# Kernel tuning notes

Hardware: AMD Instinct MI355X
Metric: run time of the kernel (lower is better)

## Reference

```python
import math
import jax, jax.numpy as jnp
import numpy as np

B = 128          # graphs per batch
N = 1024         # nodes per graph
E = 1048576      # total edges (avg degree 8)
F_IN = 64
NHID = 64
NCLS = 10
RATIO = 0.8


def setup_inputs() -> dict:
    key = jax.random.key(0)
    ks = jax.random.split(key, 24)
    x = jax.random.normal(ks[0], (B * N, F_IN), jnp.float32)
    # intra-graph random edges: graph id per edge, local src/dst
    epg = E // B
    gid = jnp.repeat(jnp.arange(B, dtype=jnp.int32), epg)
    src = gid * N + jax.random.randint(ks[1], (E,), 0, N, jnp.int32)
    dst = gid * N + jax.random.randint(ks[2], (E,), 0, N, jnp.int32)
    def lin(k, fi, fo):
        s = 1.0 / np.sqrt(fi)
        return jax.random.uniform(k, (fi, fo), jnp.float32, -s, s)
    p = {
        'W1': lin(ks[3], F_IN, NHID), 'b1': jnp.zeros((NHID,), jnp.float32),
        'Wp1': lin(ks[4], NHID, 1), 'bp1': jnp.zeros((1,), jnp.float32),
        'W2': lin(ks[5], NHID, NHID), 'b2': jnp.zeros((NHID,), jnp.float32),
        'Wp2': lin(ks[6], NHID, 1), 'bp2': jnp.zeros((1,), jnp.float32),
        'W3': lin(ks[7], NHID, NHID), 'b3': jnp.zeros((NHID,), jnp.float32),
        'Wp3': lin(ks[8], NHID, 1), 'bp3': jnp.zeros((1,), jnp.float32),
        'L1w': lin(ks[9], 2 * NHID, NHID), 'L1b': jnp.zeros((NHID,), jnp.float32),
        'L2w': lin(ks[10], NHID, NHID // 2), 'L2b': jnp.zeros((NHID // 2,), jnp.float32),
        'L3w': lin(ks[11], NHID // 2, NCLS), 'L3b': jnp.zeros((NCLS,), jnp.float32),
    }
    return dict(x=x, edge_src=src, edge_dst=dst, **p)


def gcn_conv(x, W, b, src, dst, emask, n):
    # PyG GCNConv: add self loops, symmetric deg normalization
    xw = x @ W
    ew = emask.astype(x.dtype)
    deg = jax.ops.segment_sum(ew, dst, num_segments=n) + 1.0  # +1 self loop
    dis = jax.lax.rsqrt(deg)
    norm = dis[src] * dis[dst] * ew
    agg = jax.ops.segment_sum(xw[src] * norm[:, None], dst, num_segments=n)
    agg = agg + xw * (dis * dis)[:, None]  # self-loop message
    return agg + b


def sag_pool(x, Wp, bp, src, dst, emask, n_cur):
    n_tot = B * n_cur
    k = int(math.ceil(RATIO * n_cur))
    score = gcn_conv(x, Wp, bp, src, dst, emask, n_tot)[:, 0]
    _, idx = jax.lax.top_k(score.reshape(B, n_cur), k)
    perm = (idx + (jnp.arange(B, dtype=jnp.int32) * n_cur)[:, None]).reshape(-1)
    xn = x[perm] * jnp.tanh(score[perm])[:, None]
    new_idx = jnp.full((n_tot,), -1, jnp.int32).at[perm].set(
        jnp.arange(B * k, dtype=jnp.int32))
    ns, nd = new_idx[src], new_idx[dst]
    valid = emask & (ns >= 0) & (nd >= 0)
    return xn, jnp.where(valid, ns, 0), jnp.where(valid, nd, 0), valid, k


def readout(x, k):
    xr = x.reshape(B, k, NHID)
    return jnp.concatenate([xr.max(axis=1), xr.mean(axis=1)], axis=1)


def reference(x, edge_src, edge_dst, W1, b1, Wp1, bp1, W2, b2, Wp2, bp2,
              W3, b3, Wp3, bp3, L1w, L1b, L2w, L2b, L3w, L3b):
    src = edge_src.astype(jnp.int32)
    dst = edge_dst.astype(jnp.int32)
    emask = jnp.ones((E,), bool)
    n = N
    h = jax.nn.relu(gcn_conv(x, W1, b1, src, dst, emask, B * n))
    h, src, dst, emask, n = sag_pool(h, Wp1, bp1, src, dst, emask, n)
    r1 = readout(h, n)
    h = jax.nn.relu(gcn_conv(h, W2, b2, src, dst, emask, B * n))
    h, src, dst, emask, n = sag_pool(h, Wp2, bp2, src, dst, emask, n)
    r2 = readout(h, n)
    h = jax.nn.relu(gcn_conv(h, W3, b3, src, dst, emask, B * n))
    h, src, dst, emask, n = sag_pool(h, Wp3, bp3, src, dst, emask, n)
    r3 = readout(h, n)
    z = r1 + r2 + r3
    z = jax.nn.relu(z @ L1w + L1b)          # dropout is identity in eval
    z = jax.nn.relu(z @ L2w + L2b)
    return jax.nn.log_softmax(z @ L3w + L3b, axis=-1)
```

## Files before the change

### kernel.cpp

```cpp
#include <hip/hip_runtime.h>
#include <math.h>

constexpr int B_   = 128;
constexpr int N_   = 1024;
constexpr int E_   = 1048576;
constexpr int BN_  = B_ * N_;
constexpr int EPG  = E_ / B_;
constexpr int SRT2 = EPG + 3 * 1024;
constexpr int NSEG = 16;

typedef short v8s __attribute__((ext_vector_type(8)));
typedef float v4f __attribute__((ext_vector_type(4)));

__device__ __forceinline__ unsigned bf16_rne(unsigned u) {
    return (u + 0x7FFFu + ((u >> 16) & 1u)) >> 16;
}

__global__ __launch_bounds__(1024) void k_csr2(
        const int* __restrict__ src, const int* __restrict__ dst,
        const int* __restrict__ cum,
        int* __restrict__ srt, int* __restrict__ rowptr,
        float* __restrict__ dis, int n) {
    __shared__ int cnt[1024];
    __shared__ int cur[1024];
    __shared__ int cums[1024];
    __shared__ int wsum[17];
    int g = blockIdx.x, tid = threadIdx.x;
    int gb   = g * N_;
    int base = g * n;
    const int eb = g * EPG;
    int* gsrt = srt + (size_t)g * SRT2;

    cums[tid] = cum ? cum[gb + tid] : tid;
    cnt[tid] = 0;
    __syncthreads();
    for (int t = tid; t < EPG; t += 1024) {
        int s = cums[src[eb + t] - gb];
        int d = cums[dst[eb + t] - gb];
        if ((s | d) >= 0) atomicAdd(&cnt[d], 1);
    }
    __syncthreads();

    int c  = (tid < n) ? cnt[tid] : 0;
    int pc = (c + 3) & ~3;
    int v = pc;
    int lane = tid & 63, wv = tid >> 6;
    #pragma unroll
    for (int off = 1; off < 64; off <<= 1) {
        int t = __shfl_up(v, off, 64);
        if (lane >= off) v += t;
    }
    if (lane == 63) wsum[wv] = v;
    __syncthreads();
    if (tid == 0) {
        int run = 0;
        #pragma unroll
        for (int i = 0; i < 16; ++i) { int t = wsum[i]; wsum[i] = run; run += t; }
        wsum[16] = run;
    }
    __syncthreads();
    int excl = v - pc + wsum[wv];
    if (tid < n) {
        cur[tid] = excl;
        rowptr[g * (n + 1) + tid] = excl;
        dis[base + tid] = rsqrtf((float)c + 1.0f);
    }
    if (tid == 0) rowptr[g * (n + 1) + n] = wsum[16];
    __syncthreads();

    for (int t = tid; t < EPG; t += 1024) {
        int s = cums[src[eb + t] - gb];
        int d = cums[dst[eb + t] - gb];
        if ((s | d) < 0) continue;
        int pos = atomicAdd(&cur[d], 1);
        gsrt[pos] = s;
    }
    __syncthreads();

    if (tid < n) {
        int e1 = excl + pc;
        for (int t = cur[tid]; t < e1; ++t) gsrt[t] = n;
    }
}

__global__ __launch_bounds__(1024) void k_wprep3(
        const float* __restrict__ W0, const float* __restrict__ W1,
        const float* __restrict__ W2, unsigned short* __restrict__ wfall) {
    const float* W = (blockIdx.x == 0) ? W0 : (blockIdx.x == 1) ? W1 : W2;
    unsigned short* wf = wfall + (size_t)blockIdx.x * 8192;
    int t = threadIdx.x;
    int l  = t & 63;
    int kk = (t >> 6) & 1;
    int c  = (t >> 7) & 3;
    int p  = (t >> 9) & 1;
    int col = c * 16 + (l & 15);
    int kbase = kk * 32 + (l >> 4) * 8;
    unsigned short o[8];
    #pragma unroll
    for (int j = 0; j < 8; ++j) {
        float w = W[(kbase + j) * 64 + col];
        unsigned u  = __float_as_uint(w);
        unsigned hi = bf16_rne(u);
        if (p == 0) o[j] = (unsigned short)hi;
        else {
            float lo = w - __uint_as_float(hi << 16);
            o[j] = (unsigned short)bf16_rne(__float_as_uint(lo));
        }
    }
    uint4 v;
    v.x = o[0] | ((unsigned)o[1] << 16);
    v.y = o[2] | ((unsigned)o[3] << 16);
    v.z = o[4] | ((unsigned)o[5] << 16);
    v.w = o[6] | ((unsigned)o[7] << 16);
    *reinterpret_cast<uint4*>(wf + (size_t)t * 8) = v;
}

__global__ __launch_bounds__(256) void k_xw_mfma(
        const float* __restrict__ h, const int* __restrict__ perm,
        const float* __restrict__ ggate, const unsigned short* __restrict__ wf,
        const float* __restrict__ dis, float* __restrict__ xwq, int rows) {
    __shared__ float hs[128][68];
    __shared__ float sdis[128];
    __shared__ int   lperm[128];
    __shared__ float lgate[128];
    int tid = threadIdx.x;
    int r0 = blockIdx.x * 128;

    if (perm) {
        if (tid < 128) { lperm[tid] = perm[r0 + tid]; lgate[tid] = ggate[r0 + tid]; }
        __syncthreads();
        for (int i = tid; i < 128 * 16; i += 256) {
            int row = i >> 4, s = i & 15;
            float4 v = *reinterpret_cast<const float4*>(h + (size_t)lperm[row] * 64 + s * 4);
            float gt = lgate[row];
            v.x *= gt; v.y *= gt; v.z *= gt; v.w *= gt;
            *reinterpret_cast<float4*>(&hs[row][s * 4]) = v;
        }
    } else {
        for (int i = tid; i < 128 * 16; i += 256) {
            int row = i >> 4, s = i & 15;
            float4 v = *reinterpret_cast<const float4*>(h + (size_t)(r0 + row) * 64 + s * 4);
            *reinterpret_cast<float4*>(&hs[row][s * 4]) = v;
        }
    }
    if (tid < 128) sdis[tid] = dis[r0 + tid];

    int lane = tid & 63;
    v8s wh[4][2], wl[4][2];
    #pragma unroll
    for (int c = 0; c < 4; ++c) {
        #pragma unroll
        for (int kk = 0; kk < 2; ++kk) {
            wh[c][kk] = *reinterpret_cast<const v8s*>(wf + (((size_t)((0*4 + c)*2 + kk))*64 + lane)*8);
            wl[c][kk] = *reinterpret_cast<const v8s*>(wf + (((size_t)((1*4 + c)*2 + kk))*64 + lane)*8);
        }
    }
    __syncthreads();

    int wave = tid >> 6;
    int m = lane & 15, b = lane >> 4;
    #pragma unroll
    for (int t = 0; t < 2; ++t) {
        int lr0 = (wave * 2 + t) * 16;
        float f[16];
        *reinterpret_cast<float4*>(f)      = *reinterpret_cast<const float4*>(&hs[lr0 + m][b * 8]);
        *reinterpret_cast<float4*>(f + 4)  = *reinterpret_cast<const float4*>(&hs[lr0 + m][b * 8 + 4]);
        *reinterpret_cast<float4*>(f + 8)  = *reinterpret_cast<const float4*>(&hs[lr0 + m][32 + b * 8]);
        *reinterpret_cast<float4*>(f + 12) = *reinterpret_cast<const float4*>(&hs[lr0 + m][32 + b * 8 + 4]);
        v8s ah[2], al[2];
        #pragma unroll
        for (int ch = 0; ch < 2; ++ch) {
            #pragma unroll
            for (int j = 0; j < 8; ++j) {
                float x = f[ch * 8 + j];
                unsigned u  = __float_as_uint(x);
                unsigned hi = bf16_rne(u);
                float lo = x - __uint_as_float(hi << 16);
                ah[ch][j] = (short)hi;
                al[ch][j] = (short)bf16_rne(__float_as_uint(lo));
            }
        }
        float dv[4];
        #pragma unroll
        for (int reg = 0; reg < 4; ++reg) dv[reg] = sdis[lr0 + b * 4 + reg];

        #pragma unroll
        for (int c = 0; c < 4; ++c) {
            v4f acc = {0.f, 0.f, 0.f, 0.f};
            acc = __builtin_amdgcn_mfma_f32_16x16x32_bf16(ah[0], wh[c][0], acc, 0, 0, 0);
            acc = __builtin_amdgcn_mfma_f32_16x16x32_bf16(ah[1], wh[c][1], acc, 0, 0, 0);
            acc = __builtin_amdgcn_mfma_f32_16x16x32_bf16(al[0], wh[c][0], acc, 0, 0, 0);
            acc = __builtin_amdgcn_mfma_f32_16x16x32_bf16(al[1], wh[c][1], acc, 0, 0, 0);
            acc = __builtin_amdgcn_mfma_f32_16x16x32_bf16(ah[0], wl[c][0], acc, 0, 0, 0);
            acc = __builtin_amdgcn_mfma_f32_16x16x32_bf16(ah[1], wl[c][1], acc, 0, 0, 0);
            acc = __builtin_amdgcn_mfma_f32_16x16x32_bf16(al[0], wl[c][0], acc, 0, 0, 0);
            acc = __builtin_amdgcn_mfma_f32_16x16x32_bf16(al[1], wl[c][1], acc, 0, 0, 0);
            #pragma unroll
            for (int reg = 0; reg < 4; ++reg) {
                int grow = r0 + lr0 + b * 4 + reg;
                xwq[((size_t)c * rows + grow) * 16 + m] = acc[reg] * dv[reg];
            }
        }
    }
}

__global__ __launch_bounds__(1024, 1) void k_agg_csr(
        const int* __restrict__ srt, const int* __restrict__ rowptr,
        const float* __restrict__ dis, const float* __restrict__ xwq,
        const float* __restrict__ bias, const float* __restrict__ Wp,
        float* __restrict__ hout, float* __restrict__ saggq,
        int n, int rows) {
    extern __shared__ float xs[];
    int lrpPad = (n + 4) & ~3;
    int* lrp  = (int*)(xs + (n + 1) * 20);
    int* lsrt = lrp + lrpPad;

    int g = blockIdx.x & 127, q = blockIdx.x >> 7;
    int foff = q * 16;
    int tid  = threadIdx.x;
    int base = g * n;
    const float* plane = xwq + ((size_t)q * rows + base) * 16;

    for (int i = tid; i < n * 4; i += 1024) {
        int row = i >> 2, sub = i & 3;
        float4 v = *reinterpret_cast<const float4*>(plane + row * 16 + sub * 4);
        *reinterpret_cast<float4*>(xs + row * 20 + sub * 4) = v;
    }
    if (tid < 20) xs[n * 20 + tid] = 0.0f;
    for (int i = tid; i <= n; i += 1024) lrp[i] = rowptr[g * (n + 1) + i];
    __syncthreads();
    int total = lrp[n];
    const int* gsrt = srt + (size_t)g * SRT2;
    for (int i = tid; i < total; i += 1024) lsrt[i] = gsrt[i];
    __syncthreads();

    int sub = tid & 3;
    float4 bq  = *reinterpret_cast<const float4*>(bias + foff + sub * 4);
    float4 wp4 = *reinterpret_cast<const float4*>(Wp   + foff + sub * 4);
    for (int row = tid >> 2; row < n; row += 256) {
        int s0 = lrp[row], s1 = lrp[row + 1];
        float4 acc = *reinterpret_cast<const float4*>(xs + row * 20 + sub * 4);
        for (int j = s0; j < s1; j += 4) {
            int4 nb = *reinterpret_cast<const int4*>(lsrt + j);
            const float4 v0 = *reinterpret_cast<const float4*>(xs + nb.x * 20 + sub * 4);
            const float4 v1 = *reinterpret_cast<const float4*>(xs + nb.y * 20 + sub * 4);
            const float4 v2 = *reinterpret_cast<const float4*>(xs + nb.z * 20 + sub * 4);
            const float4 v3 = *reinterpret_cast<const float4*>(xs + nb.w * 20 + sub * 4);
            acc.x += v0.x + v1.x + v2.x + v3.x;
            acc.y += v0.y + v1.y + v2.y + v3.y;
            acc.z += v0.z + v1.z + v2.z + v3.z;
            acc.w += v0.w + v1.w + v2.w + v3.w;
        }
        float dsc = dis[base + row];
        float4 o;
        o.x = fmaxf(fmaf(dsc, acc.x, bq.x), 0.0f);
        o.y = fmaxf(fmaf(dsc, acc.y, bq.y), 0.0f);
        o.z = fmaxf(fmaf(dsc, acc.z, bq.z), 0.0f);
        o.w = fmaxf(fmaf(dsc, acc.w, bq.w), 0.0f);
        *reinterpret_cast<float4*>(hout + (size_t)(base + row) * 64 + foff + sub * 4) = o;
        float part = o.x * wp4.x + o.y * wp4.y + o.z * wp4.z + o.w * wp4.w;
        part += __shfl_xor(part, 1, 64);
        part += __shfl_xor(part, 2, 64);
        if (sub == 0) xs[row * 20 + 16] = part * dsc;
    }
    __syncthreads();

    for (int row = tid; row < n; row += 1024) {
        float acc = xs[row * 20 + 16];
        int s1 = lrp[row + 1];
        for (int j = lrp[row]; j < s1; j += 4) {
            int4 nb = *reinterpret_cast<const int4*>(lsrt + j);
            acc += xs[nb.x * 20 + 16] + xs[nb.y * 20 + 16]
                 + xs[nb.z * 20 + 16] + xs[nb.w * 20 + 16];
        }
        saggq[(size_t)q * BN_ + base + row] = acc;
    }
}

__global__ __launch_bounds__(1024) void k_score_topk(
        const float* __restrict__ dis, const float* __restrict__ saggq,
        const float* __restrict__ bp, int n, int k,
        int* __restrict__ perm, float* __restrict__ ggate,
        int* __restrict__ cum, int do_compose) {
    __shared__ unsigned long long keys[1024];
    __shared__ int mark[1024];
    int g = blockIdx.x, tid = threadIdx.x;
    int base = g * n;
    float bp0 = bp[0];

    unsigned long long kv = 0ull;
    if (tid < n) {
        float s0 = saggq[0 * (size_t)BN_ + base + tid] + saggq[1 * (size_t)BN_ + base + tid]
                 + saggq[2 * (size_t)BN_ + base + tid] + saggq[3 * (size_t)BN_ + base + tid];
        float sag = dis[base + tid] * s0 + bp0;
        unsigned u  = __float_as_uint(sag);
        unsigned mk = (u & 0x80000000u) ? ~u : (u | 0x80000000u);
        kv = ((unsigned long long)mk << 32) | (unsigned)tid;
    }
    keys[tid] = kv;
    mark[tid] = -1;

    for (int size = 2; size <= 1024; size <<= 1) {
        for (int stride = size >> 1; stride > 0; stride >>= 1) {
            __syncthreads();
            if (tid < 512) {
                int a  = ((tid / stride) * (stride << 1)) + (tid & (stride - 1));
                int bx = a + stride;
                bool asc = ((a & size) == 0);
                unsigned long long ka = keys[a], kb = keys[bx];
                bool sw = asc ? (ka > kb) : (ka < kb);
                if (sw) { keys[a] = kb; keys[bx] = ka; }
            }
        }
    }
    __syncthreads();

    if (tid < k) {
        int j = tid;
        unsigned long long kvv = keys[1023 - j];
        int local   = (int)(kvv & 0xFFFFFFFFull);
        unsigned mk = (unsigned)(kvv >> 32);
        unsigned u  = (mk & 0x80000000u) ? (mk ^ 0x80000000u) : ~mk;
        int newg = g * k + j;
        perm[newg]  = base + local;
        ggate[newg] = tanhf(__uint_as_float(u));
        mark[local] = j;
    }
    __syncthreads();
    if (do_compose) {
        int gb = g * N_;
        int c = (do_compose == 1) ? tid : cum[gb + tid];
        cum[gb + tid] = (c >= 0) ? mark[c] : -1;
    }
}

__global__ __launch_bounds__(256) void k_readout_seg(
        const float* __restrict__ h, const int* __restrict__ perm,
        const float* __restrict__ ggate, int k, float* __restrict__ pz) {
    int g = blockIdx.x / NSEG, seg = blockIdx.x % NSEG;
    int ck = (k + NSEG - 1) / NSEG;
    int j0 = seg * ck;
    int j1 = min(k, j0 + ck);
    __shared__ float gate[64];
    __shared__ int   lperm[64];
    int tid = threadIdx.x;
    for (int j = j0 + tid; j < j1; j += 256) {
        lperm[j - j0] = perm[g * k + j];
        gate[j - j0]  = ggate[g * k + j];
    }
    __syncthreads();
    int lane = tid & 63, w = tid >> 6;
    float mx = -INFINITY, sm = 0.0f;
    for (int j = j0 + w; j < j1; j += 4) {
        float v = h[(size_t)lperm[j - j0] * 64 + lane] * gate[j - j0];
        mx = fmaxf(mx, v); sm += v;
    }
    __shared__ float smx[4][64], ssm[4][64];
    smx[w][lane] = mx; ssm[w][lane] = sm;
    __syncthreads();
    if (w == 0) {
        #pragma unroll
        for (int i = 1; i < 4; ++i) { mx = fmaxf(mx, smx[i][lane]); sm += ssm[i][lane]; }
        float* p = pz + ((size_t)g * NSEG + seg) * 128;
        p[lane]      = mx;
        p[64 + lane] = sm;
    }
}

__global__ __launch_bounds__(128) void k_mlp(const float* __restrict__ pz,
                      const float* __restrict__ L1w, const float* __restrict__ L1b,
                      const float* __restrict__ L2w, const float* __restrict__ L2b,
                      const float* __restrict__ L3w, const float* __restrict__ L3b,
                      float* __restrict__ out) {
    __shared__ float z[128], h1[64], h2[32], lg[10], lse;
    int g = blockIdx.x, tid = threadIdx.x;
    const float kinv[3] = {1.0f / 820.0f, 1.0f / 656.0f, 1.0f / 525.0f};
    float zv = 0.0f;
    if (tid < 64) {
        #pragma unroll
        for (int L = 0; L < 3; ++L) {
            const float* p = pz + (((size_t)L * B_ + g) * NSEG) * 128;
            float mx = -INFINITY;
            #pragma unroll
            for (int s = 0; s < NSEG; ++s) mx = fmaxf(mx, p[s * 128 + tid]);
            zv += mx;
        }
    } else {
        int f = tid - 64;
        #pragma unroll
        for (int L = 0; L < 3; ++L) {
            const float* p = pz + (((size_t)L * B_ + g) * NSEG) * 128;
            float sm = 0.0f;
            #pragma unroll
            for (int s = 0; s < NSEG; ++s) sm += p[s * 128 + 64 + f];
            zv += sm * kinv[L];
        }
    }
    z[tid] = zv;
    __syncthreads();
    if (tid < 64) {
        float acc = L1b[tid];
        for (int i = 0; i < 128; ++i) acc = fmaf(z[i], L1w[i * 64 + tid], acc);
        h1[tid] = fmaxf(acc, 0.0f);
    }
    __syncthreads();
    if (tid < 32) {
        float acc = L2b[tid];
        for (int i = 0; i < 64; ++i) acc = fmaf(h1[i], L2w[i * 32 + tid], acc);
        h2[tid] = fmaxf(acc, 0.0f);
    }
    __syncthreads();
    if (tid < 10) {
        float acc = L3b[tid];
        for (int i = 0; i < 32; ++i) acc = fmaf(h2[i], L3w[i * 10 + tid], acc);
        lg[tid] = acc;
    }
    __syncthreads();
    if (tid == 0) {
        float m = lg[0];
        for (int i = 1; i < 10; ++i) m = fmaxf(m, lg[i]);
        float s = 0.0f;
        for (int i = 0; i < 10; ++i) s += expf(lg[i] - m);
        lse = m + logf(s);
    }
    __syncthreads();
    if (tid < 10) out[g * 10 + tid] = lg[tid] - lse;
}

extern "C" void kernel_launch(void* const* d_in, const int* in_sizes, int n_in,
                              void* d_out, int out_size, void* d_ws, size_t ws_size,
                              hipStream_t stream) {
    const float* x    = (const float*)d_in[0];
    const int*   esrc = (const int*)d_in[1];
    const int*   edst = (const int*)d_in[2];
    const float* W [3] = {(const float*)d_in[3],  (const float*)d_in[7],  (const float*)d_in[11]};
    const float* bb[3] = {(const float*)d_in[4],  (const float*)d_in[8],  (const float*)d_in[12]};
    const float* Wp[3] = {(const float*)d_in[5],  (const float*)d_in[9],  (const float*)d_in[13]};
    const float* bp[3] = {(const float*)d_in[6],  (const float*)d_in[10], (const float*)d_in[14]};
    const float* L1w = (const float*)d_in[15];
    const float* L1b = (const float*)d_in[16];
    const float* L2w = (const float*)d_in[17];
    const float* L2b = (const float*)d_in[18];
    const float* L3w = (const float*)d_in[19];
    const float* L3b = (const float*)d_in[20];
    float* out = (float*)d_out;

    float* fws   = (float*)d_ws;
    float* agg   = fws;
    float* xwq   = agg  + (size_t)BN_ * 64;
    float* dis   = xwq  + (size_t)BN_ * 64;
    float* saggq = dis  + BN_;
    float* ggate = saggq + 4 * (size_t)BN_;
    float* pz    = ggate + BN_;
    int*   perm   = (int*)(pz + 3 * B_ * NSEG * 128);
    int*   cum    = perm + BN_;
    int*   srt    = cum + BN_;
    int*   rowptr = srt + (size_t)B_ * SRT2;
    unsigned short* wfrag = (unsigned short*)(rowptr + B_ * (N_ + 1));

    hipFuncSetAttribute(reinterpret_cast<const void*>(k_agg_csr),
                        hipFuncAttributeMaxDynamicSharedMemorySize,
                        (1025 * 20 + 1028 + SRT2) * 4);

    k_wprep3<<<3, 1024, 0, stream>>>(W[0], W[1], W[2], wfrag);

    const int ks_[3] = {820, 656, 525};
    int n = N_;

    for (int L = 0; L < 3; ++L) {
        int rows = B_ * n;
        int k    = ks_[L];

        k_csr2<<<B_, 1024, 0, stream>>>(esrc, edst, (L == 0) ? nullptr : cum,
                                        srt, rowptr, dis, n);

        if (L == 0)
            k_xw_mfma<<<rows / 128, 256, 0, stream>>>(x, nullptr, nullptr,
                                                      wfrag, dis, xwq, rows);
        else
            k_xw_mfma<<<rows / 128, 256, 0, stream>>>(agg, perm, ggate,
                                                      wfrag + (size_t)L * 8192, dis, xwq, rows);

        int lrpPad = (n + 4) & ~3;
        k_agg_csr<<<B_ * 4, 1024, (size_t)((n + 1) * 20 + lrpPad + SRT2) * 4, stream>>>(
            srt, rowptr, dis, xwq, bb[L], Wp[L], agg, saggq, n, rows);

        k_score_topk<<<B_, 1024, 0, stream>>>(dis, saggq, bp[L], n, k,
                                              perm, ggate, cum, (L < 2) ? (L + 1) : 0);

        k_readout_seg<<<B_ * NSEG, 256, 0, stream>>>(agg, perm, ggate, k,
                                                     pz + (size_t)L * B_ * NSEG * 128);

        n = k;
    }

    k_mlp<<<B_, 128, 0, stream>>>(pz, L1w, L1b, L2w, L2b, L3w, L3b, out);
}
```

Measured before the change: 262.1 us.

## Split CSR aggregation into eight 8-feature slices with 16-bit neighbor indices

The aggregation kernel now launches 8 blocks per graph, each owning 8 feature columns instead of 16, which cuts the per-block LDS feature tile from 20 to 12 floats per row. Neighbor indices are stored in LDS as unsigned shorts, halving that buffer. The smaller footprint is meant to let more blocks share a CU and to add parallelism. The cost is that each block reloads the whole edge list and row pointers, and the score partial sums grow from 4 to 8 planes, so the top-k kernel reads twice as many.

```diff
diff --git a/kernel.cpp b/kernel.cpp
--- a/kernel.cpp
+++ b/kernel.cpp
@@ -204,48 +204,49 @@
     }
 }
 
-__global__ __launch_bounds__(1024, 1) void k_agg_csr(
+__global__ __launch_bounds__(1024, 8) void k_agg8(
         const int* __restrict__ srt, const int* __restrict__ rowptr,
         const float* __restrict__ dis, const float* __restrict__ xwq,
         const float* __restrict__ bias, const float* __restrict__ Wp,
-        float* __restrict__ hout, float* __restrict__ saggq,
+        float* __restrict__ hout, float* __restrict__ sagg8,
         int n, int rows) {
     extern __shared__ float xs[];
     int lrpPad = (n + 4) & ~3;
-    int* lrp  = (int*)(xs + (n + 1) * 20);
-    int* lsrt = lrp + lrpPad;
-
-    int g = blockIdx.x & 127, q = blockIdx.x >> 7;
-    int foff = q * 16;
+    int* lrp = (int*)(xs + (n + 1) * 12);
+    unsigned short* lsrtU = (unsigned short*)(lrp + lrpPad);
+
+    int g = blockIdx.x & 127, e8 = blockIdx.x >> 7;
+    int q = e8 >> 1, half = (e8 & 1) * 8;
+    int foff = q * 16 + half;
     int tid  = threadIdx.x;
     int base = g * n;
-    const float* plane = xwq + ((size_t)q * rows + base) * 16;
-
-    for (int i = tid; i < n * 4; i += 1024) {
-        int row = i >> 2, sub = i & 3;
-        float4 v = *reinterpret_cast<const float4*>(plane + row * 16 + sub * 4);
-        *reinterpret_cast<float4*>(xs + row * 20 + sub * 4) = v;
-    }
-    if (tid < 20) xs[n * 20 + tid] = 0.0f;
+    const float* plane = xwq + ((size_t)q * rows + base) * 16 + half;
+
+    for (int i = tid; i < n * 2; i += 1024) {
+        int row = i >> 1, s = i & 1;
+        float4 v = *reinterpret_cast<const float4*>(plane + row * 16 + s * 4);
+        *reinterpret_cast<float4*>(xs + row * 12 + s * 4) = v;
+    }
+    if (tid < 12) xs[n * 12 + tid] = 0.0f;
     for (int i = tid; i <= n; i += 1024) lrp[i] = rowptr[g * (n + 1) + i];
     __syncthreads();
     int total = lrp[n];
     const int* gsrt = srt + (size_t)g * SRT2;
-    for (int i = tid; i < total; i += 1024) lsrt[i] = gsrt[i];
-    __syncthreads();
-
-    int sub = tid & 3;
+    for (int i = tid; i < total; i += 1024) lsrtU[i] = (unsigned short)gsrt[i];
+    __syncthreads();
+
+    int sub = tid & 1;
     float4 bq  = *reinterpret_cast<const float4*>(bias + foff + sub * 4);
     float4 wp4 = *reinterpret_cast<const float4*>(Wp   + foff + sub * 4);
-    for (int row = tid >> 2; row < n; row += 256) {
+    for (int row = tid >> 1; row < n; row += 512) {
         int s0 = lrp[row], s1 = lrp[row + 1];
-        float4 acc = *reinterpret_cast<const float4*>(xs + row * 20 + sub * 4);
+        float4 acc = *reinterpret_cast<const float4*>(xs + row * 12 + sub * 4);
         for (int j = s0; j < s1; j += 4) {
-            int4 nb = *reinterpret_cast<const int4*>(lsrt + j);
-            const float4 v0 = *reinterpret_cast<const float4*>(xs + nb.x * 20 + sub * 4);
-            const float4 v1 = *reinterpret_cast<const float4*>(xs + nb.y * 20 + sub * 4);
-            const float4 v2 = *reinterpret_cast<const float4*>(xs + nb.z * 20 + sub * 4);
-            const float4 v3 = *reinterpret_cast<const float4*>(xs + nb.w * 20 + sub * 4);
+            ushort4 nb = *reinterpret_cast<const ushort4*>(lsrtU + j);
+            const float4 v0 = *reinterpret_cast<const float4*>(xs + nb.x * 12 + sub * 4);
+            const float4 v1 = *reinterpret_cast<const float4*>(xs + nb.y * 12 + sub * 4);
+            const float4 v2 = *reinterpret_cast<const float4*>(xs + nb.z * 12 + sub * 4);
+            const float4 v3 = *reinterpret_cast<const float4*>(xs + nb.w * 12 + sub * 4);
             acc.x += v0.x + v1.x + v2.x + v3.x;
             acc.y += v0.y + v1.y + v2.y + v3.y;
             acc.z += v0.z + v1.z + v2.z + v3.z;
@@ -260,25 +261,24 @@
         *reinterpret_cast<float4*>(hout + (size_t)(base + row) * 64 + foff + sub * 4) = o;
         float part = o.x * wp4.x + o.y * wp4.y + o.z * wp4.z + o.w * wp4.w;
         part += __shfl_xor(part, 1, 64);
-        part += __shfl_xor(part, 2, 64);
-        if (sub == 0) xs[row * 20 + 16] = part * dsc;
+        if (sub == 0) xs[row * 12 + 8] = part * dsc;
     }
     __syncthreads();
 
     for (int row = tid; row < n; row += 1024) {
-        float acc = xs[row * 20 + 16];
+        float acc = xs[row * 12 + 8];
         int s1 = lrp[row + 1];
         for (int j = lrp[row]; j < s1; j += 4) {
-            int4 nb = *reinterpret_cast<const int4*>(lsrt + j);
-            acc += xs[nb.x * 20 + 16] + xs[nb.y * 20 + 16]
-                 + xs[nb.z * 20 + 16] + xs[nb.w * 20 + 16];
-        }
-        saggq[(size_t)q * BN_ + base + row] = acc;
+            ushort4 nb = *reinterpret_cast<const ushort4*>(lsrtU + j);
+            acc += xs[nb.x * 12 + 8] + xs[nb.y * 12 + 8]
+                 + xs[nb.z * 12 + 8] + xs[nb.w * 12 + 8];
+        }
+        sagg8[(size_t)e8 * BN_ + base + row] = acc;
     }
 }
 
 __global__ __launch_bounds__(1024) void k_score_topk(
-        const float* __restrict__ dis, const float* __restrict__ saggq,
+        const float* __restrict__ dis, const float* __restrict__ sagg8,
         const float* __restrict__ bp, int n, int k,
         int* __restrict__ perm, float* __restrict__ ggate,
         int* __restrict__ cum, int do_compose) {
@@ -290,8 +290,9 @@
 
     unsigned long long kv = 0ull;
     if (tid < n) {
-        float s0 = saggq[0 * (size_t)BN_ + base + tid] + saggq[1 * (size_t)BN_ + base + tid]
-                 + saggq[2 * (size_t)BN_ + base + tid] + saggq[3 * (size_t)BN_ + base + tid];
+        float s0 = 0.0f;
+        #pragma unroll
+        for (int p = 0; p < 8; ++p) s0 += sagg8[(size_t)p * BN_ + base + tid];
         float sag = dis[base + tid] * s0 + bp0;
         unsigned u  = __float_as_uint(sag);
         unsigned mk = (u & 0x80000000u) ? ~u : (u | 0x80000000u);
@@ -449,8 +450,8 @@
     float* agg   = fws;
     float* xwq   = agg  + (size_t)BN_ * 64;
     float* dis   = xwq  + (size_t)BN_ * 64;
-    float* saggq = dis  + BN_;
-    float* ggate = saggq + 4 * (size_t)BN_;
+    float* sagg8 = dis  + BN_;
+    float* ggate = sagg8 + 8 * (size_t)BN_;
     float* pz    = ggate + BN_;
     int*   perm   = (int*)(pz + 3 * B_ * NSEG * 128);
     int*   cum    = perm + BN_;
@@ -458,9 +459,9 @@
     int*   rowptr = srt + (size_t)B_ * SRT2;
     unsigned short* wfrag = (unsigned short*)(rowptr + B_ * (N_ + 1));
 
-    hipFuncSetAttribute(reinterpret_cast<const void*>(k_agg_csr),
+    hipFuncSetAttribute(reinterpret_cast<const void*>(k_agg8),
                         hipFuncAttributeMaxDynamicSharedMemorySize,
-                        (1025 * 20 + 1028 + SRT2) * 4);
+                        1025 * 12 * 4 + 1028 * 4 + SRT2 * 2);
 
     k_wprep3<<<3, 1024, 0, stream>>>(W[0], W[1], W[2], wfrag);
 
@@ -482,10 +483,11 @@
                                                       wfrag + (size_t)L * 8192, dis, xwq, rows);
 
         int lrpPad = (n + 4) & ~3;
-        k_agg_csr<<<B_ * 4, 1024, (size_t)((n + 1) * 20 + lrpPad + SRT2) * 4, stream>>>(
-            srt, rowptr, dis, xwq, bb[L], Wp[L], agg, saggq, n, rows);
-
-        k_score_topk<<<B_, 1024, 0, stream>>>(dis, saggq, bp[L], n, k,
+        size_t ldsB = (size_t)(n + 1) * 12 * 4 + (size_t)lrpPad * 4 + (size_t)SRT2 * 2;
+        k_agg8<<<B_ * 8, 1024, ldsB, stream>>>(
+            srt, rowptr, dis, xwq, bb[L], Wp[L], agg, sagg8, n, rows);
+
+        k_score_topk<<<B_, 1024, 0, stream>>>(dis, sagg8, bp[L], n, k,
                                               perm, ggate, cum, (L < 2) ? (L + 1) : 0);
 
         k_readout_seg<<<B_ * NSEG, 256, 0, stream>>>(agg, perm, ggate, k,
```

New measurement: 264.6 us. Within noise of the previous version (+1.0%).
